# Kernel optimization log

Measured on AMD Instinct MI355X. Metric: run time of the kernel, lower is better.

Reference implementation:

```python
import jax, jax.numpy as jnp
import numpy as np

HEADS = 4
DIM_HEAD = 32
DIM = 128
HIDDEN = HEADS * DIM_HEAD  # 128


def setup_inputs() -> dict:
    key = jax.random.key(0)
    k1, k2, k3 = jax.random.split(key, 3)
    B, C, H, W = 16, DIM, 128, 128
    x = jax.random.normal(k1, (B, C, H, W), dtype=jnp.float32)
    # 1x1 convs are pointwise channel mixes: weight [out_ch, in_ch]
    w_qkv = jax.random.normal(k2, (3 * HIDDEN, C), dtype=jnp.float32) * 0.05
    w_out = jax.random.normal(k3, (DIM, HIDDEN), dtype=jnp.float32) * 0.05
    b_out = jnp.zeros((DIM,), dtype=jnp.float32)
    return {"x": x, "w_qkv": w_qkv, "w_out": w_out, "b_out": b_out}


def reference(x, w_qkv, w_out, b_out):
    b, c, H, W = x.shape
    n = H * W
    scale = DIM_HEAD ** -0.5
    # to_qkv: 1x1 conv == channel GEMM -> [b, 3*hidden, n], then split (tf.split axis=1)
    qkv = jnp.einsum('oc,bchw->bohw', w_qkv, x).reshape(b, 3, HEADS, DIM_HEAD, n)
    q, k, v = qkv[:, 0], qkv[:, 1], qkv[:, 2]  # each [b, h, d, n]
    q = q * scale
    k = jax.nn.softmax(k, axis=-1)  # softmax over spatial tokens n
    context = jnp.einsum('bhdn,bhen->bhde', k, v)   # [b, h, d, e], small d x e
    out = jnp.einsum('bhde,bhdn->bhen', context, q)  # [b, h, e, n]
    out = out.reshape(b, HIDDEN, H, W)
    # to_out: 1x1 conv with bias
    return jnp.einsum('oc,bchw->bohw', w_out, out) + b_out[None, :, None, None]
```

## Files before the change

### kernel.cpp

```cpp
#include <hip/hip_runtime.h>
#include <cmath>

#define NBATCH 16
#define NCH    128
#define NPIX   16384
#define NREP   2

#define WS_S_OFF 0
#define WS_A_OFF (NBATCH * NREP * 128)
#define WS_ZERO_FLOATS (WS_A_OFF + NBATCH * NREP * 4096)
#define WS_MBF_BYTE ((size_t)WS_ZERO_FLOATS * 4)

typedef __bf16 bf16x8 __attribute__((ext_vector_type(8)));
typedef __bf16 bf16x4 __attribute__((ext_vector_type(4)));
typedef __bf16 bf16x2 __attribute__((ext_vector_type(2)));
typedef float  f32x4  __attribute__((ext_vector_type(4)));

#define MFMA16(a, b, c) __builtin_amdgcn_mfma_f32_16x16x32_bf16((a), (b), (c), 0, 0, 0)

__device__ __forceinline__ void barrier_lds() {
    asm volatile("s_waitcnt lgkmcnt(0)\n\ts_barrier" ::: "memory");
}

__global__ __launch_bounds__(256, 2) void k1_partials(const float* __restrict__ x,
                                                      const float* __restrict__ w_qkv,
                                                      float* __restrict__ ws)
{
    const int b = blockIdx.y;
    const int g = blockIdx.x;
    const int t = threadIdx.x;
    const int w = t >> 6;
    const int l = t & 63;
    const int lm = l & 15;
    const int q  = l >> 4;

    __shared__ __align__(16) __bf16 Xs[64][136];
    __shared__ __align__(16) __bf16 EVs[256][40];

    const float* wkv = w_qkv + 128 * NCH;
    bf16x8 wfrag[4][4];
#pragma unroll
    for (int rt = 0; rt < 4; ++rt) {
        const int row = (rt < 2) ? (w * 32 + rt * 16 + lm)
                                 : (128 + w * 32 + (rt - 2) * 16 + lm);
#pragma unroll
        for (int ks = 0; ks < 4; ++ks) {
            const float* src = wkv + row * NCH + ks * 32 + q * 8;
            float4 p0 = *(const float4*)src;
            float4 p1 = *(const float4*)(src + 4);
            bf16x8 f;
            f[0] = (__bf16)p0.x; f[1] = (__bf16)p0.y; f[2] = (__bf16)p0.z; f[3] = (__bf16)p0.w;
            f[4] = (__bf16)p1.x; f[5] = (__bf16)p1.y; f[6] = (__bf16)p1.z; f[7] = (__bf16)p1.w;
            wfrag[rt][ks] = f;
        }
    }

    f32x4 a_acc[2][2];
#pragma unroll
    for (int dt = 0; dt < 2; ++dt)
#pragma unroll
        for (int et = 0; et < 2; ++et) a_acc[dt][et] = (f32x4)0.f;
    float s8[8];
#pragma unroll
    for (int j = 0; j < 8; ++j) s8[j] = 0.f;

    float fx[8][4];
    const float* xbase = x + (size_t)(b * NCH + w * 32) * NPIX + l;

    {
        const int n0 = g * 64;
#pragma unroll
        for (int rq = 0; rq < 8; ++rq) {
            const float* xb = xbase + (size_t)(rq * 4) * NPIX + n0;
            fx[rq][0] = xb[0];
            fx[rq][1] = xb[NPIX];
            fx[rq][2] = xb[2 * NPIX];
            fx[rq][3] = xb[3 * NPIX];
        }
    }

    for (int ci = 0; ci < 8; ++ci) {
#pragma unroll
        for (int rq = 0; rq < 8; ++rq) {
            bf16x4 pk;
            pk[0] = (__bf16)fx[rq][0]; pk[1] = (__bf16)fx[rq][1];
            pk[2] = (__bf16)fx[rq][2]; pk[3] = (__bf16)fx[rq][3];
            *(bf16x4*)&Xs[l][w * 32 + rq * 4] = pk;
        }
        if (ci < 7) {
            const int n0 = (g + (ci + 1) * 32) * 64;
#pragma unroll
            for (int rq = 0; rq < 8; ++rq) {
                const float* xb = xbase + (size_t)(rq * 4) * NPIX + n0;
                fx[rq][0] = xb[0];
                fx[rq][1] = xb[NPIX];
                fx[rq][2] = xb[2 * NPIX];
                fx[rq][3] = xb[3 * NPIX];
            }
        }
        barrier_lds();

        f32x4 acc[4][4];
#pragma unroll
        for (int rt = 0; rt < 4; ++rt)
#pragma unroll
            for (int ct = 0; ct < 4; ++ct) acc[rt][ct] = (f32x4)0.f;

#pragma unroll
        for (int ks = 0; ks < 4; ++ks) {
            bf16x8 bf[4];
#pragma unroll
            for (int ct = 0; ct < 4; ++ct)
                bf[ct] = *(const bf16x8*)&Xs[ct * 16 + lm][ks * 32 + q * 8];
#pragma unroll
            for (int rt = 0; rt < 4; ++rt)
#pragma unroll
                for (int ct = 0; ct < 4; ++ct)
                    acc[rt][ct] = MFMA16(wfrag[rt][ks], bf[ct], acc[rt][ct]);
        }

#pragma unroll
        for (int hf = 0; hf < 2; ++hf) {
#pragma unroll
            for (int rt = 0; rt < 4; ++rt) {
                const int rowbase = (rt < 2) ? (w * 32 + rt * 16)
                                             : (128 + w * 32 + (rt - 2) * 16);
#pragma unroll
                for (int c2 = 0; c2 < 2; ++c2) {
                    const int ct = hf * 2 + c2;
                    f32x4 v = acc[rt][ct];
                    if (rt < 2) {
#pragma unroll
                        for (int r = 0; r < 4; ++r) {
                            float e = __expf(v[r]);
                            v[r] = e;
                            s8[rt * 4 + r] += e;
                        }
                    }
                    const int colw = c2 * 16 + (lm & ~1);
#pragma unroll
                    for (int s = 0; s < 2; ++s) {
                        float fe = v[2 * s];
                        float fo = v[2 * s + 1];
                        float ge = __shfl_xor(fe, 1);
                        float go = __shfl_xor(fo, 1);
                        bf16x2 pw;
                        if (l & 1) { pw[0] = (__bf16)go; pw[1] = (__bf16)fo; }
                        else       { pw[0] = (__bf16)fe; pw[1] = (__bf16)ge; }
                        const int roww = rowbase + q * 4 + 2 * s + (l & 1);
                        *(bf16x2*)&EVs[roww][colw] = pw;
                    }
                }
            }
            {
                bf16x8 ea[2], vb[2];
#pragma unroll
                for (int dt = 0; dt < 2; ++dt)
                    ea[dt] = *(const bf16x8*)&EVs[w * 32 + dt * 16 + lm][q * 8];
#pragma unroll
                for (int et = 0; et < 2; ++et)
                    vb[et] = *(const bf16x8*)&EVs[128 + w * 32 + et * 16 + lm][q * 8];
#pragma unroll
                for (int dt = 0; dt < 2; ++dt)
#pragma unroll
                    for (int et = 0; et < 2; ++et)
                        a_acc[dt][et] = MFMA16(ea[dt], vb[et], a_acc[dt][et]);
            }
        }
        barrier_lds();
    }

    const int rep = g & (NREP - 1);

#pragma unroll
    for (int j = 0; j < 8; ++j) {
        float v = s8[j];
        v += __shfl_xor(v, 1);
        v += __shfl_xor(v, 2);
        v += __shfl_xor(v, 4);
        v += __shfl_xor(v, 8);
        s8[j] = v;
    }
    if (lm == 0) {
        float* Sp = ws + WS_S_OFF + (size_t)(b * NREP + rep) * 128;
#pragma unroll
        for (int rt2 = 0; rt2 < 2; ++rt2)
#pragma unroll
            for (int r = 0; r < 4; ++r)
                atomicAdd(&Sp[w * 32 + rt2 * 16 + q * 4 + r], s8[rt2 * 4 + r]);
    }
    {
        float* Ab = ws + WS_A_OFF + (size_t)((b * NREP + rep) * 4 + w) * 1024;
#pragma unroll
        for (int dt = 0; dt < 2; ++dt)
#pragma unroll
            for (int et = 0; et < 2; ++et)
#pragma unroll
                for (int r = 0; r < 4; ++r)
                    atomicAdd(&Ab[(dt * 16 + q * 4 + r) * 32 + et * 16 + lm],
                              a_acc[dt][et][r]);
    }
}

__global__ __launch_bounds__(256) void k2_mprime(const float* __restrict__ w_qkv,
                                                 const float* __restrict__ w_out,
                                                 const float* __restrict__ ws,
                                                 __bf16* __restrict__ Mbf)
{
    const int b  = blockIdx.x;
    const int o0 = blockIdx.y * 32;
    const int t  = threadIdx.x;

    __shared__ float ctx[4][32][32];
    __shared__ float Ts[32][128];
    __shared__ float Wqs[32][128];
    __shared__ float Ss[128];

    if (t < 128) {
        float s = 0.f;
#pragma unroll
        for (int r = 0; r < NREP; ++r)
            s += ws[WS_S_OFF + (size_t)(b * NREP + r) * 128 + t];
        Ss[t] = s;
    }
    __syncthreads();

    for (int i = t; i < 4096; i += 256) {
        float a = 0.f;
#pragma unroll
        for (int r = 0; r < NREP; ++r)
            a += ws[WS_A_OFF + (size_t)(b * NREP + r) * 4096 + i];
        const int hh = i >> 10, d = (i >> 5) & 31, e = i & 31;
        ctx[hh][d][e] = a / Ss[hh * 32 + d];
    }
    __syncthreads();

    {
        const int oo  = t >> 3;
        const int o   = o0 + oo;
        const int hd0 = (t & 7) * 16;
        const int hh  = hd0 >> 5;
        const int db  = hd0 & 31;
        float wo[32];
#pragma unroll
        for (int e4 = 0; e4 < 32; e4 += 4)
            *(float4*)&wo[e4] = *(const float4*)&w_out[o * NCH + hh * 32 + e4];
#pragma unroll
        for (int k = 0; k < 16; ++k) {
            const int d = db + k;
            float s = 0.f;
#pragma unroll
            for (int e = 0; e < 32; ++e) s = fmaf(wo[e], ctx[hh][d][e], s);
            Ts[oo][hd0 + k] = s;
        }
    }
    __syncthreads();

    float macc[16];
#pragma unroll
    for (int ii = 0; ii < 16; ++ii) macc[ii] = 0.f;

    for (int slab = 0; slab < 4; ++slab) {
        for (int i = t; i < 32 * 128; i += 256)
            Wqs[i >> 7][i & 127] = w_qkv[(size_t)(slab * 32 + (i >> 7)) * NCH + (i & 127)];
        __syncthreads();
#pragma unroll
        for (int ii = 0; ii < 16; ++ii) {
            const int i  = t + ii * 256;
            const int oo = i >> 7;
            const int c  = i & 127;
            float s = macc[ii];
#pragma unroll
            for (int k = 0; k < 32; ++k)
                s = fmaf(Ts[oo][slab * 32 + k], Wqs[k][c], s);
            macc[ii] = s;
        }
        __syncthreads();
    }

    const float scale = 0.17677669529663687f;
#pragma unroll
    for (int ii = 0; ii < 16; ++ii) {
        const int i  = t + ii * 256;
        const int oo = i >> 7;
        const int c  = i & 127;
        Mbf[(size_t)(b * NCH + o0 + oo) * NCH + c] = (__bf16)(macc[ii] * scale);
    }
}

__global__ __launch_bounds__(256, 4) void k3_out(const float* __restrict__ x,
                                                 const float* __restrict__ bias,
                                                 const __bf16* __restrict__ Mbf,
                                                 float* __restrict__ y)
{
    const int b  = blockIdx.y;
    const int n0 = blockIdx.x * 64;
    const int t  = threadIdx.x;
    const int w  = t >> 6, l = t & 63;
    const int lm = l & 15, q = l >> 4;

    __shared__ __align__(16) __bf16 Xs[64][136];

    const __bf16* Mb = Mbf + (size_t)b * NCH * NCH;
    bf16x8 mfrag[2][4];
#pragma unroll
    for (int rt = 0; rt < 2; ++rt)
#pragma unroll
        for (int ks = 0; ks < 4; ++ks)
            mfrag[rt][ks] = *(const bf16x8*)&Mb[(size_t)(w * 32 + rt * 16 + lm) * NCH + ks * 32 + q * 8];

#pragma unroll
    for (int rq = 0; rq < 8; ++rq) {
        const int r0 = w * 32 + rq * 4;
        const float* xb = x + (size_t)(b * NCH + r0) * NPIX + n0 + l;
        float f0 = xb[0], f1 = xb[NPIX], f2 = xb[2 * NPIX], f3 = xb[3 * NPIX];
        bf16x4 pk;
        pk[0] = (__bf16)f0; pk[1] = (__bf16)f1; pk[2] = (__bf16)f2; pk[3] = (__bf16)f3;
        *(bf16x4*)&Xs[l][r0] = pk;
    }
    __syncthreads();

    f32x4 acc[2][4];
#pragma unroll
    for (int rt = 0; rt < 2; ++rt)
#pragma unroll
        for (int ct = 0; ct < 4; ++ct) acc[rt][ct] = (f32x4)0.f;

#pragma unroll
    for (int ks = 0; ks < 4; ++ks) {
        bf16x8 bf[4];
#pragma unroll
        for (int ct = 0; ct < 4; ++ct)
            bf[ct] = *(const bf16x8*)&Xs[ct * 16 + lm][ks * 32 + q * 8];
#pragma unroll
        for (int rt = 0; rt < 2; ++rt)
#pragma unroll
            for (int ct = 0; ct < 4; ++ct)
                acc[rt][ct] = MFMA16(mfrag[rt][ks], bf[ct], acc[rt][ct]);
    }

#pragma unroll
    for (int rt = 0; rt < 2; ++rt) {
#pragma unroll
        for (int r = 0; r < 4; ++r) {
            const int row = w * 32 + rt * 16 + q * 4 + r;
            const float bb = bias[row];
            float* yp = y + (size_t)(b * NCH + row) * NPIX + n0 + lm;
#pragma unroll
            for (int ct = 0; ct < 4; ++ct)
                yp[ct * 16] = acc[rt][ct][r] + bb;
        }
    }
}

extern "C" void kernel_launch(void* const* d_in, const int* in_sizes, int n_in,
                              void* d_out, int out_size, void* d_ws, size_t ws_size,
                              hipStream_t stream) {
    (void)in_sizes; (void)n_in; (void)out_size; (void)ws_size;
    const float* x     = (const float*)d_in[0];
    const float* w_qkv = (const float*)d_in[1];
    const float* w_out = (const float*)d_in[2];
    const float* b_out = (const float*)d_in[3];
    float*  y   = (float*)d_out;
    float*  ws  = (float*)d_ws;
    __bf16* Mbf = (__bf16*)((char*)d_ws + WS_MBF_BYTE);

    hipMemsetAsync(d_ws, 0, (size_t)WS_ZERO_FLOATS * 4, stream);

    k1_partials<<<dim3(32, NBATCH),        256, 0, stream>>>(x, w_qkv, ws);
    k2_mprime  <<<dim3(NBATCH, 4),         256, 0, stream>>>(w_qkv, w_out, ws, Mbf);
    k3_out     <<<dim3(NPIX / 64, NBATCH), 256, 0, stream>>>(x, b_out, Mbf, y);
}
```

Measured before the change: 323.8 us.

## Replace atomic partial reduction with per-block slots and restructure LDS staging

Each k1 block now writes its softmax sums and context partials to its own workspace slot with plain stores instead of atomicAdd into two replicas. This removes the memset launch and atomic contention. k2 then sums all 32 slots per batch. The LDS staging of exp(k) and v is also reorganised into per-wave interleaved column pairs, which removes the lane shuffles used to pack bf16 pairs. In exchange, k2 does 16x more workspace reads and the workspace grows.

```diff
diff --git a/kernel.cpp b/kernel.cpp
--- a/kernel.cpp
+++ b/kernel.cpp
@@ -4,12 +4,12 @@
 #define NBATCH 16
 #define NCH    128
 #define NPIX   16384
-#define NREP   2
+#define NSLOT  32
 
 #define WS_S_OFF 0
-#define WS_A_OFF (NBATCH * NREP * 128)
-#define WS_ZERO_FLOATS (WS_A_OFF + NBATCH * NREP * 4096)
-#define WS_MBF_BYTE ((size_t)WS_ZERO_FLOATS * 4)
+#define WS_A_OFF (NBATCH * NSLOT * 128)
+#define WS_TOT_FLOATS (WS_A_OFF + NBATCH * NSLOT * 4096)
+#define WS_MBF_BYTE ((size_t)WS_TOT_FLOATS * 4)
 
 typedef __bf16 bf16x8 __attribute__((ext_vector_type(8)));
 typedef __bf16 bf16x4 __attribute__((ext_vector_type(4)));
@@ -35,7 +35,8 @@
     const int q  = l >> 4;
 
     __shared__ __align__(16) __bf16 Xs[64][136];
-    __shared__ __align__(16) __bf16 EVs[256][40];
+    __shared__ __align__(16) __bf16 Ee[4][32][20][2];
+    __shared__ __align__(16) __bf16 Vv[4][32][20][2];
 
     const float* wkv = w_qkv + 128 * NCH;
     bf16x8 wfrag[4][4];
@@ -122,44 +123,36 @@
 #pragma unroll
         for (int hf = 0; hf < 2; ++hf) {
 #pragma unroll
-            for (int rt = 0; rt < 4; ++rt) {
-                const int rowbase = (rt < 2) ? (w * 32 + rt * 16)
-                                             : (128 + w * 32 + (rt - 2) * 16);
-#pragma unroll
-                for (int c2 = 0; c2 < 2; ++c2) {
-                    const int ct = hf * 2 + c2;
-                    f32x4 v = acc[rt][ct];
-                    if (rt < 2) {
-#pragma unroll
-                        for (int r = 0; r < 4; ++r) {
-                            float e = __expf(v[r]);
-                            v[r] = e;
-                            s8[rt * 4 + r] += e;
-                        }
-                    }
-                    const int colw = c2 * 16 + (lm & ~1);
-#pragma unroll
-                    for (int s = 0; s < 2; ++s) {
-                        float fe = v[2 * s];
-                        float fo = v[2 * s + 1];
-                        float ge = __shfl_xor(fe, 1);
-                        float go = __shfl_xor(fo, 1);
-                        bf16x2 pw;
-                        if (l & 1) { pw[0] = (__bf16)go; pw[1] = (__bf16)fo; }
-                        else       { pw[0] = (__bf16)fe; pw[1] = (__bf16)ge; }
-                        const int roww = rowbase + q * 4 + 2 * s + (l & 1);
-                        *(bf16x2*)&EVs[roww][colw] = pw;
-                    }
+            for (int rt = 0; rt < 2; ++rt) {
+                f32x4 v0 = acc[rt][hf * 2 + 0];
+                f32x4 v1 = acc[rt][hf * 2 + 1];
+#pragma unroll
+                for (int r = 0; r < 4; ++r) {
+                    float e0 = __expf(v0[r]);
+                    float e1 = __expf(v1[r]);
+                    s8[rt * 4 + r] += e0 + e1;
+                    bf16x2 pw; pw[0] = (__bf16)e0; pw[1] = (__bf16)e1;
+                    *(bf16x2*)&Ee[w][rt * 16 + q * 4 + r][lm][0] = pw;
+                }
+            }
+#pragma unroll
+            for (int rt = 0; rt < 2; ++rt) {
+                f32x4 v0 = acc[rt + 2][hf * 2 + 0];
+                f32x4 v1 = acc[rt + 2][hf * 2 + 1];
+#pragma unroll
+                for (int r = 0; r < 4; ++r) {
+                    bf16x2 pw; pw[0] = (__bf16)v0[r]; pw[1] = (__bf16)v1[r];
+                    *(bf16x2*)&Vv[w][rt * 16 + q * 4 + r][lm][0] = pw;
                 }
             }
             {
                 bf16x8 ea[2], vb[2];
 #pragma unroll
                 for (int dt = 0; dt < 2; ++dt)
-                    ea[dt] = *(const bf16x8*)&EVs[w * 32 + dt * 16 + lm][q * 8];
+                    ea[dt] = *(const bf16x8*)&Ee[w][dt * 16 + lm][q * 4][0];
 #pragma unroll
                 for (int et = 0; et < 2; ++et)
-                    vb[et] = *(const bf16x8*)&EVs[128 + w * 32 + et * 16 + lm][q * 8];
+                    vb[et] = *(const bf16x8*)&Vv[w][et * 16 + lm][q * 4][0];
 #pragma unroll
                 for (int dt = 0; dt < 2; ++dt)
 #pragma unroll
@@ -169,8 +162,6 @@
         }
         barrier_lds();
     }
-
-    const int rep = g & (NREP - 1);
 
 #pragma unroll
     for (int j = 0; j < 8; ++j) {
@@ -182,23 +173,22 @@
         s8[j] = v;
     }
     if (lm == 0) {
-        float* Sp = ws + WS_S_OFF + (size_t)(b * NREP + rep) * 128;
+        float* Sp = ws + WS_S_OFF + (size_t)(b * NSLOT + g) * 128;
 #pragma unroll
         for (int rt2 = 0; rt2 < 2; ++rt2)
 #pragma unroll
             for (int r = 0; r < 4; ++r)
-                atomicAdd(&Sp[w * 32 + rt2 * 16 + q * 4 + r], s8[rt2 * 4 + r]);
+                Sp[w * 32 + rt2 * 16 + q * 4 + r] = s8[rt2 * 4 + r];
     }
     {
-        float* Ab = ws + WS_A_OFF + (size_t)((b * NREP + rep) * 4 + w) * 1024;
+        float* Ab = ws + WS_A_OFF + (size_t)((b * NSLOT + g) * 4 + w) * 1024;
 #pragma unroll
         for (int dt = 0; dt < 2; ++dt)
 #pragma unroll
             for (int et = 0; et < 2; ++et)
 #pragma unroll
                 for (int r = 0; r < 4; ++r)
-                    atomicAdd(&Ab[(dt * 16 + q * 4 + r) * 32 + et * 16 + lm],
-                              a_acc[dt][et][r]);
+                    Ab[(dt * 16 + q * 4 + r) * 32 + et * 16 + lm] = a_acc[dt][et][r];
     }
 }
 
@@ -219,8 +209,8 @@
     if (t < 128) {
         float s = 0.f;
 #pragma unroll
-        for (int r = 0; r < NREP; ++r)
-            s += ws[WS_S_OFF + (size_t)(b * NREP + r) * 128 + t];
+        for (int r = 0; r < NSLOT; ++r)
+            s += ws[WS_S_OFF + (size_t)(b * NSLOT + r) * 128 + t];
         Ss[t] = s;
     }
     __syncthreads();
@@ -228,8 +218,8 @@
     for (int i = t; i < 4096; i += 256) {
         float a = 0.f;
 #pragma unroll
-        for (int r = 0; r < NREP; ++r)
-            a += ws[WS_A_OFF + (size_t)(b * NREP + r) * 4096 + i];
+        for (int r = 0; r < NSLOT; ++r)
+            a += ws[WS_A_OFF + (size_t)(b * NSLOT + r) * 4096 + i];
         const int hh = i >> 10, d = (i >> 5) & 31, e = i & 31;
         ctx[hh][d][e] = a / Ss[hh * 32 + d];
     }
@@ -365,9 +355,7 @@
     float*  ws  = (float*)d_ws;
     __bf16* Mbf = (__bf16*)((char*)d_ws + WS_MBF_BYTE);
 
-    hipMemsetAsync(d_ws, 0, (size_t)WS_ZERO_FLOATS * 4, stream);
-
-    k1_partials<<<dim3(32, NBATCH),        256, 0, stream>>>(x, w_qkv, ws);
+    k1_partials<<<dim3(NSLOT, NBATCH),     256, 0, stream>>>(x, w_qkv, ws);
     k2_mprime  <<<dim3(NBATCH, 4),         256, 0, stream>>>(w_qkv, w_out, ws, Mbf);
     k3_out     <<<dim3(NPIX / 64, NBATCH), 256, 0, stream>>>(x, b_out, Mbf, y);
 }
```

Measured after the change: 326.7 us. Within noise of the previous version (+0.9%).
